# Optimization experiments

Hardware: AMD Instinct MI355X
Metric: run time of the kernel (lower is better)

Reference implementation:

```python
import jax, jax.numpy as jnp
import numpy as np

TOP_K = 5
EPS = 1e-12

def _l2norm(x, axis=-1):
    n = jnp.sqrt(jnp.sum(x * x, axis=axis, keepdims=True))
    return x / jnp.maximum(n, EPS)

def setup_inputs() -> dict:
    key = jax.random.key(0)
    ks = jax.random.split(key, 6)
    B, S, D, N = 16, 2048, 512, 200000
    return {
        "hidden_states": jax.random.normal(ks[0], (B, S, D), dtype=jnp.float32),
        "doc_embeddings": jax.random.normal(ks[1], (N, D), dtype=jnp.float32),
        "W_q": jax.random.normal(ks[2], (D, D), dtype=jnp.float32) * 0.02,
        "b_q": jnp.zeros((D,), dtype=jnp.float32),
        "W_gate": jax.random.normal(ks[3], (D, 2 * D), dtype=jnp.float32) * 0.02,
        "b_gate": jnp.zeros((D,), dtype=jnp.float32),
    }

def reference(hidden_states, doc_embeddings, W_q, b_q, W_gate, b_gate):
    B, S, D = hidden_states.shape
    # set_doc_embeddings: cosine metric normalizes doc table once
    docs = _l2norm(doc_embeddings, axis=1)          # [N, D]
    # forward: mean-pool query, linear encode
    query = hidden_states.mean(axis=1)              # [B, D]
    query = query @ W_q.T + b_q                     # torch Linear: x @ W^T + b
    # cosine similarity scan over full corpus
    q = _l2norm(query, axis=1)                      # [B, D]
    scores_full = q @ docs.T                        # [B, N]  (memory-bound scan)
    top_scores, indices = jax.lax.top_k(scores_full, TOP_K)  # [B, K], [B, K]
    # fuse context (gate method)
    retrieved = docs[indices]                       # [B, K, D] gather
    weights = jax.nn.softmax(top_scores, axis=1)    # [B, K]
    context = jnp.einsum('bk,bkd->bd', weights, retrieved)   # [B, D]
    context_exp = jnp.broadcast_to(context[:, None, :], (B, S, D))
    combined = jnp.concatenate([hidden_states, context_exp], axis=-1)  # [B, S, 2D]
    gate = jax.nn.sigmoid(combined @ W_gate.T + b_gate)       # [B, S, D]
    fused = gate * hidden_states + (1.0 - gate) * context_exp
    return top_scores, indices, fused
```

## Files before the change

kernel.cpp:

```cpp
#include <hip/hip_runtime.h>
#include <hip/hip_bf16.h>
#include <math.h>

#define BB 16
#define SS 2048
#define DD 512
#define NDOCS 200000
#define TOPK 5
#define EPSN 1e-12f
#define NEG_INF (-3.0e38f)

#define NB3 782
#define NW3 (NB3 * 4)
#define NT3 (NDOCS / 16)
#define QSTR 520

typedef short s16x8 __attribute__((ext_vector_type(8)));
typedef float f32x4 __attribute__((ext_vector_type(4)));

__device__ __forceinline__ short f2bf(float f) {
    __bf16 b = (__bf16)f;
    short s;
    __builtin_memcpy(&s, &b, 2);
    return s;
}

__device__ __forceinline__ void gload_lds16(const void* g, void* l) {
    __builtin_amdgcn_global_load_lds(
        (const __attribute__((address_space(1))) void*)g,
        (__attribute__((address_space(3))) void*)l, 16, 0, 0);
}

__global__ __launch_bounds__(128) void k1_mean_partial(
    const float* __restrict__ hs, float* __restrict__ partial) {
    int b = blockIdx.y, sc = blockIdx.x;
    int t = threadIdx.x;
    const float4* src = (const float4*)(hs + (size_t)(b * SS + sc * 64) * DD);
    float4 acc = {0.f, 0.f, 0.f, 0.f};
    for (int s = 0; s < 64; ++s) {
        float4 v = src[(size_t)s * 128 + t];
        acc.x += v.x; acc.y += v.y; acc.z += v.z; acc.w += v.w;
    }
    ((float4*)partial)[(size_t)(sc * BB + b) * 128 + t] = acc;
}

__global__ __launch_bounds__(128) void k1b_mean_reduce(
    const float* __restrict__ partial, float* __restrict__ mean) {
    int b = blockIdx.y, jc = blockIdx.x;
    int j = jc * 128 + threadIdx.x;
    float s = 0.f;
    for (int c = 0; c < 32; ++c) s += partial[(size_t)(c * BB + b) * DD + j];
    mean[(size_t)b * DD + j] = s * (1.0f / 2048.0f);
}

__global__ __launch_bounds__(256) void k2a_q_gemv(
    const float* __restrict__ mean, const float* __restrict__ Wq,
    const float* __restrict__ bq, float* __restrict__ qtmp) {
    int b = blockIdx.y, jc = blockIdx.x;
    int t = threadIdx.x;
    int r = t >> 4, c = t & 15;
    int row = jc * 16 + r;
    const float4* wr = (const float4*)(Wq + (size_t)row * DD);
    const float4* mv = (const float4*)(mean + (size_t)b * DD);
    float acc = 0.f;
#pragma unroll
    for (int it = 0; it < 8; ++it) {
        int k4 = c + it * 16;
        float4 w = wr[k4], m = mv[k4];
        acc = fmaf(w.x, m.x, acc); acc = fmaf(w.y, m.y, acc);
        acc = fmaf(w.z, m.z, acc); acc = fmaf(w.w, m.w, acc);
    }
#pragma unroll
    for (int m = 1; m < 16; m <<= 1) acc += __shfl_xor(acc, m);
    if (c == 0) qtmp[(size_t)b * DD + row] = acc + bq[row];
}

__global__ __launch_bounds__(256) void k2b_q_norm(
    const float* __restrict__ qtmp, float* __restrict__ qv) {
    int b = blockIdx.x, t = threadIdx.x;
    __shared__ float red[4];
    float a0 = qtmp[(size_t)b * DD + t];
    float a1 = qtmp[(size_t)b * DD + t + 256];
    float ss = a0 * a0 + a1 * a1;
#pragma unroll
    for (int m = 1; m < 64; m <<= 1) ss += __shfl_xor(ss, m);
    if ((t & 63) == 0) red[t >> 6] = ss;
    __syncthreads();
    float inv = 1.0f / fmaxf(sqrtf(red[0] + red[1] + red[2] + red[3]), EPSN);
    qv[(size_t)b * DD + t] = a0 * inv;
    qv[(size_t)b * DD + t + 256] = a1 * inv;
}

__global__ __launch_bounds__(256) void k3_scores(
    const float* __restrict__ docs, const float* __restrict__ qv,
    float* __restrict__ cand_s, int* __restrict__ cand_i) {
    __shared__ short qS[2][BB * QSTR];

    int t = threadIdx.x;
    int w = t >> 6, lane = t & 63;
    int bq = lane & 15, kg = lane >> 4;

    for (int u = t; u < BB * DD; u += 256) {
        int b = u >> 9, k = u & 511;
        float f = qv[u];
        unsigned uu = __float_as_uint(f);
        qS[0][b * QSTR + k] = (short)(uu >> 16);
        qS[1][b * QSTR + k] = f2bf(f - __uint_as_float(uu & 0xFFFF0000u));
    }
    __syncthreads();

    int gw = blockIdx.x * 4 + w;

    float lv[TOPK]; int li[TOPK];
#pragma unroll
    for (int r = 0; r < TOPK; ++r) { lv[r] = NEG_INF; li[r] = 0x7fffffff; }

    auto ins = [&](float s, int di) {
        if (s > lv[4] || (s == lv[4] && di < li[4])) {
            lv[4] = s; li[4] = di;
#pragma unroll
            for (int k = 4; k > 0; --k) {
                if (lv[k] > lv[k - 1] || (lv[k] == lv[k - 1] && li[k] < li[k - 1])) {
                    float tv = lv[k]; lv[k] = lv[k - 1]; lv[k - 1] = tv;
                    int   ti = li[k]; li[k] = li[k - 1]; li[k - 1] = ti;
                }
            }
        }
    };

    const short* qh_base = &qS[0][bq * QSTR + kg * 8];
    const short* ql_base = &qS[1][bq * QSTR + kg * 8];

    long tt = gw;
    const float* dpt = docs + ((long)tt * 16 + bq) * DD + kg * 8;
    f32x4 A0 = *(const f32x4*)(dpt);
    f32x4 A1 = *(const f32x4*)(dpt + 4);
    f32x4 B0 = *(const f32x4*)(dpt + 32);
    f32x4 B1 = *(const f32x4*)(dpt + 36);

    while (tt < NT3) {
        long tt2 = (tt + NW3 < NT3) ? tt + NW3 : tt;
        const float* dpn = docs + (tt2 * 16 + bq) * DD + kg * 8;

        f32x4 acc1 = {0.f, 0.f, 0.f, 0.f};
        f32x4 acc2 = {0.f, 0.f, 0.f, 0.f};
        float nrm = 0.f;

#pragma unroll
        for (int c = 0; c < 16; ++c) {
            f32x4 C0, C1;
            if (c + 2 < 16) {
                C0 = *(const f32x4*)(dpt + (c + 2) * 32);
                C1 = *(const f32x4*)(dpt + (c + 2) * 32 + 4);
            } else {
                C0 = *(const f32x4*)(dpn + (c - 14) * 32);
                C1 = *(const f32x4*)(dpn + (c - 14) * 32 + 4);
            }
            float ef[8] = {A0[0], A0[1], A0[2], A0[3], A1[0], A1[1], A1[2], A1[3]};
            s16x8 ah, al;
#pragma unroll
            for (int i = 0; i < 8; ++i) {
                unsigned u = __float_as_uint(ef[i]);
                ah[i] = (short)(u >> 16);
                al[i] = f2bf(ef[i] - __uint_as_float(u & 0xFFFF0000u));
                nrm = fmaf(ef[i], ef[i], nrm);
            }
            s16x8 qh = *(const s16x8*)(qh_base + c * 32);
            s16x8 ql = *(const s16x8*)(ql_base + c * 32);
            acc1 = __builtin_amdgcn_mfma_f32_16x16x32_bf16(ah, qh, acc1, 0, 0, 0);
            acc2 = __builtin_amdgcn_mfma_f32_16x16x32_bf16(ah, ql, acc2, 0, 0, 0);
            acc2 = __builtin_amdgcn_mfma_f32_16x16x32_bf16(al, qh, acc2, 0, 0, 0);
            A0 = B0; A1 = B1; B0 = C0; B1 = C1;
        }

        float nn = nrm + __shfl_xor(nrm, 16);
        nn += __shfl_xor(nn, 32);
        float invn = 1.0f / fmaxf(sqrtf(nn), EPSN);
        f32x4 acct = acc1 + acc2;
#pragma unroll
        for (int r = 0; r < 4; ++r) {
            float iv = __shfl(invn, kg * 4 + r);
            ins(acct[r] * iv, (int)(tt * 16 + kg * 4 + r));
        }

        tt += NW3;
        dpt = dpn;
    }

#pragma unroll
    for (int step = 16; step <= 32; step <<= 1) {
        float ov[TOPK]; int oi[TOPK];
#pragma unroll
        for (int r = 0; r < TOPK; ++r) {
            ov[r] = __shfl_xor(lv[r], step);
            oi[r] = __shfl_xor(li[r], step);
        }
#pragma unroll
        for (int r = 0; r < TOPK; ++r) ins(ov[r], oi[r]);
    }

    if (kg == 0) {
#pragma unroll
        for (int r = 0; r < TOPK; ++r) {
            cand_s[((long)gw * BB + bq) * TOPK + r] = lv[r];
            cand_i[((long)gw * BB + bq) * TOPK + r] = li[r];
        }
    }
}

__global__ __launch_bounds__(256) void k4a_topk_ctx(
    const float* __restrict__ docs, const float* __restrict__ cand_s,
    const int* __restrict__ cand_i, float* __restrict__ ctx,
    float* __restrict__ outp) {
    int b = blockIdx.x, t = threadIdx.x;
    __shared__ float sv[256];
    __shared__ int   si[256];
    __shared__ float topv[TOPK];
    __shared__ int   topi[TOPK];
    __shared__ float red[4];
    __shared__ float nrm5[TOPK];
    __shared__ float wts[TOPK];

    float lv[TOPK]; int li[TOPK];
#pragma unroll
    for (int r = 0; r < TOPK; ++r) { lv[r] = NEG_INF; li[r] = 0x7fffffff; }

    for (int j = t; j < NW3 * TOPK; j += 256) {
        int blk = j / TOPK, r = j - blk * TOPK;
        float s = cand_s[(long)blk * (BB * TOPK) + b * TOPK + r];
        int  di = cand_i[(long)blk * (BB * TOPK) + b * TOPK + r];
        if (s > lv[TOPK - 1] || (s == lv[TOPK - 1] && di < li[TOPK - 1])) {
            lv[TOPK - 1] = s; li[TOPK - 1] = di;
#pragma unroll
            for (int k = TOPK - 1; k > 0; --k) {
                if (lv[k] > lv[k - 1] || (lv[k] == lv[k - 1] && li[k] < li[k - 1])) {
                    float tv = lv[k]; lv[k] = lv[k - 1]; lv[k - 1] = tv;
                    int   ti = li[k]; li[k] = li[k - 1]; li[k - 1] = ti;
                }
            }
        }
    }

    int p = 0;
    for (int r = 0; r < TOPK; ++r) {
        float hv = (p < TOPK) ? lv[p] : NEG_INF;
        int   hi = (p < TOPK) ? li[p] : 0x7fffffff;
        sv[t] = hv; si[t] = hi;
        __syncthreads();
        for (int off = 128; off > 0; off >>= 1) {
            if (t < off) {
                float ov = sv[t + off]; int oi = si[t + off];
                if (ov > sv[t] || (ov == sv[t] && oi < si[t])) { sv[t] = ov; si[t] = oi; }
            }
            __syncthreads();
        }
        if (t == 0) { topv[r] = sv[0]; topi[r] = si[0]; }
        __syncthreads();
        if (hv == topv[r] && hi == topi[r]) ++p;
        __syncthreads();
    }

    for (int r = 0; r < TOPK; ++r) {
        const float* dr = docs + (size_t)topi[r] * DD;
        float s2 = dr[t] * dr[t] + dr[t + 256] * dr[t + 256];
#pragma unroll
        for (int m = 1; m < 64; m <<= 1) s2 += __shfl_xor(s2, m);
        if ((t & 63) == 0) red[t >> 6] = s2;
        __syncthreads();
        if (t == 0) nrm5[r] = sqrtf(red[0] + red[1] + red[2] + red[3]);
        __syncthreads();
    }

    if (t == 0) {
        float m = topv[0];
        float e[TOPK], s = 0.f;
#pragma unroll
        for (int r = 0; r < TOPK; ++r) { e[r] = expf(topv[r] - m); s += e[r]; }
#pragma unroll
        for (int r = 0; r < TOPK; ++r) wts[r] = e[r] / s;
    }
    __syncthreads();

    for (int j = t; j < DD; j += 256) {
        float c = 0.f;
#pragma unroll
        for (int r = 0; r < TOPK; ++r)
            c += wts[r] * docs[(size_t)topi[r] * DD + j] / fmaxf(nrm5[r], EPSN);
        ctx[(size_t)b * DD + j] = c;
    }

    if (t < TOPK) {
        outp[b * TOPK + t] = topv[t];
        outp[BB * TOPK + b * TOPK + t] = (float)topi[t];
    }
}

__global__ __launch_bounds__(256) void k4b_ctxb_gemv(
    const float* __restrict__ ctx, const float* __restrict__ Wg,
    const float* __restrict__ bgt, float* __restrict__ ctxb) {
    int b = blockIdx.y, jc = blockIdx.x;
    int t = threadIdx.x;
    int r = t >> 4, c = t & 15;
    int row = jc * 16 + r;
    const float4* wr = (const float4*)(Wg + (size_t)row * (2 * DD) + DD);
    const float4* mv = (const float4*)(ctx + (size_t)b * DD);
    float acc = 0.f;
#pragma unroll
    for (int it = 0; it < 8; ++it) {
        int k4 = c + it * 16;
        float4 w = wr[k4], m = mv[k4];
        acc = fmaf(w.x, m.x, acc); acc = fmaf(w.y, m.y, acc);
        acc = fmaf(w.z, m.z, acc); acc = fmaf(w.w, m.w, acc);
    }
#pragma unroll
    for (int m = 1; m < 16; m <<= 1) acc += __shfl_xor(acc, m);
    if (c == 0) ctxb[(size_t)b * DD + row] = acc + bgt[row];
}

#define BK 32
__global__ __launch_bounds__(512, 2) void k5_gemm_fused(
    const float* __restrict__ hs, const float* __restrict__ Wg,
    const float* __restrict__ ctx, const float* __restrict__ ctxb,
    float* __restrict__ outF) {
    __shared__ short At[128][BK];
    __shared__ short Bt[512][BK];
    __shared__ float ctxLds[DD];
    __shared__ float ctxbLds[DD];

    int bm = blockIdx.x;
    int t = threadIdx.x;
    int wv = t >> 6, lane = t & 63, ln = lane & 15, kg = lane >> 4;
    int wm = (wv >> 2) * 64, wn = (wv & 3) * 128;
    int bbatch = bm >> 4;

    ctxLds[t]  = ctx[(size_t)bbatch * DD + t];
    ctxbLds[t] = ctxb[(size_t)bbatch * DD + t];

    float4 pf[5][2];
    auto gload = [&](int kt) {
        {
            const float* src = hs + (size_t)(bm * 128 + (t >> 2)) * DD + kt * BK + (t & 3) * 8;
            pf[0][0] = ((const float4*)src)[0];
            pf[0][1] = ((const float4*)src)[1];
        }
#pragma unroll
        for (int i = 0; i < 4; ++i) {
            int u = t + i * 512;
            const float* src = Wg + (size_t)(u >> 2) * (2 * DD) + kt * BK + (u & 3) * 8;
            pf[1 + i][0] = ((const float4*)src)[0];
            pf[1 + i][1] = ((const float4*)src)[1];
        }
    };
    auto cvt1 = [&](float4 lo, float4 hi) {
        s16x8 cv;
        cv[0] = f2bf(lo.x); cv[1] = f2bf(lo.y); cv[2] = f2bf(lo.z); cv[3] = f2bf(lo.w);
        cv[4] = f2bf(hi.x); cv[5] = f2bf(hi.y); cv[6] = f2bf(hi.z); cv[7] = f2bf(hi.w);
        return cv;
    };
    auto cvtwrite = [&]() {
        {
            int row = t >> 2, slot = t & 3;
            int sl = slot ^ ((row >> 1) & 3);
            *(s16x8*)(&At[row][sl * 8]) = cvt1(pf[0][0], pf[0][1]);
        }
#pragma unroll
        for (int i = 0; i < 4; ++i) {
            int u = t + i * 512;
            int row = u >> 2, slot = u & 3;
            int sl = slot ^ ((row >> 1) & 3);
            *(s16x8*)(&Bt[row][sl * 8]) = cvt1(pf[1 + i][0], pf[1 + i][1]);
        }
    };

    f32x4 accv[4][8];
#pragma unroll
    for (int i = 0; i < 4; ++i)
#pragma unroll
        for (int j = 0; j < 8; ++j) accv[i][j] = (f32x4){0.f, 0.f, 0.f, 0.f};

    gload(0);
    for (int kt = 0; kt < DD / BK; ++kt) {
        __syncthreads();
        cvtwrite();
        if (kt + 1 < DD / BK) gload(kt + 1);
        __syncthreads();
        s16x8 af[4], bfr[8];
#pragma unroll
        for (int mi = 0; mi < 4; ++mi) {
            int row = wm + mi * 16 + ln;
            int sl = kg ^ ((row >> 1) & 3);
            af[mi] = *(const s16x8*)&At[row][sl * 8];
        }
#pragma unroll
        for (int nj = 0; nj < 8; ++nj) {
            int row = wn + nj * 16 + ln;
            int sl = kg ^ ((row >> 1) & 3);
            bfr[nj] = *(const s16x8*)&Bt[row][sl * 8];
        }
#pragma unroll
        for (int mi = 0; mi < 4; ++mi)
#pragma unroll
            for (int nj = 0; nj < 8; ++nj)
                accv[mi][nj] = __builtin_amdgcn_mfma_f32_16x16x32_bf16(
                    af[mi], bfr[nj], accv[mi][nj], 0, 0, 0);
    }

#pragma unroll
    for (int mi = 0; mi < 4; ++mi)
#pragma unroll
        for (int nj = 0; nj < 8; ++nj)
#pragma unroll
            for (int r = 0; r < 4; ++r) {
                int ri = wm + mi * 16 + kg * 4 + r;
                int ci = wn + nj * 16 + ln;
                size_t grow = (size_t)bm * 128 + ri;
                float logit = accv[mi][nj][r] + ctxbLds[ci];
                float g = __builtin_amdgcn_rcpf(1.0f + __expf(-logit));
                float h = hs[grow * DD + ci];
                float cx = ctxLds[ci];
                outF[grow * DD + ci] = g * h + (1.0f - g) * cx;
            }
}

extern "C" void kernel_launch(void* const* d_in, const int* in_sizes, int n_in,
                              void* d_out, int out_size, void* d_ws, size_t ws_size,
                              hipStream_t stream) {
    const float* hs   = (const float*)d_in[0];
    const float* docs = (const float*)d_in[1];
    const float* Wq   = (const float*)d_in[2];
    const float* bq   = (const float*)d_in[3];
    const float* Wg   = (const float*)d_in[4];
    const float* bgt  = (const float*)d_in[5];
    float* outp = (float*)d_out;
    float* ws = (float*)d_ws;

    float* partial = ws;
    float* mean    = partial + 32 * BB * DD;
    float* qtmp    = mean + BB * DD;
    float* qv      = qtmp + BB * DD;
    float* ctx     = qv + BB * DD;
    float* ctxb    = ctx + BB * DD;
    float* cand_s  = ctxb + BB * DD;
    int*   cand_i  = (int*)(cand_s + (size_t)NW3 * BB * TOPK);

    k1_mean_partial<<<dim3(32, BB), 128, 0, stream>>>(hs, partial);
    k1b_mean_reduce<<<dim3(4, BB), 128, 0, stream>>>(partial, mean);
    k2a_q_gemv<<<dim3(32, BB), 256, 0, stream>>>(mean, Wq, bq, qtmp);
    k2b_q_norm<<<BB, 256, 0, stream>>>(qtmp, qv);
    k3_scores<<<NB3, 256, 0, stream>>>(docs, qv, cand_s, cand_i);
    k4a_topk_ctx<<<BB, 256, 0, stream>>>(docs, cand_s, cand_i, ctx, outp);
    k4b_ctxb_gemv<<<dim3(32, BB), 256, 0, stream>>>(ctx, Wg, bgt, ctxb);
    k5_gemm_fused<<<256, 512, 0, stream>>>(hs, Wg, ctx, ctxb,
                                           outp + 2 * BB * TOPK);
}
```

Measured before the change: 257.3 us.

## Fuse small query/context kernels and deepen doc prefetch in score scan

Three small kernels (mean reduce, query GEMV, query norm) become one 16-block kernel, and the top-k/context kernel now also computes the context-gate GEMV, which removes three launches. The scoring kernel moves to 512-thread blocks with half as many blocks and prefetches four doc chunks ahead in a ring instead of two. The fused GEMVs run on only 16 blocks, with one thread walking a whole 2KB weight row through uncoalesced loads, so those phases may get slower even though launch overhead drops.

Result: slower. 289.0 us (+12.3%).

```diff
diff --git a/kernel.cpp b/kernel.cpp
--- a/kernel.cpp
+++ b/kernel.cpp
@@ -10,8 +10,8 @@
 #define EPSN 1e-12f
 #define NEG_INF (-3.0e38f)
 
-#define NB3 782
-#define NW3 (NB3 * 4)
+#define NB3 391
+#define NW3 (NB3 * 8)
 #define NT3 (NDOCS / 16)
 #define QSTR 520
 
@@ -23,12 +23,6 @@
     short s;
     __builtin_memcpy(&s, &b, 2);
     return s;
-}
-
-__device__ __forceinline__ void gload_lds16(const void* g, void* l) {
-    __builtin_amdgcn_global_load_lds(
-        (const __attribute__((address_space(1))) void*)g,
-        (__attribute__((address_space(3))) void*)l, 16, 0, 0);
 }
 
 __global__ __launch_bounds__(128) void k1_mean_partial(
@@ -44,54 +38,38 @@
     ((float4*)partial)[(size_t)(sc * BB + b) * 128 + t] = acc;
 }
 
-__global__ __launch_bounds__(128) void k1b_mean_reduce(
-    const float* __restrict__ partial, float* __restrict__ mean) {
-    int b = blockIdx.y, jc = blockIdx.x;
-    int j = jc * 128 + threadIdx.x;
+__global__ __launch_bounds__(512) void k2_query(
+    const float* __restrict__ partial, const float* __restrict__ Wq,
+    const float* __restrict__ bqv, float* __restrict__ qv) {
+    int b = blockIdx.x, t = threadIdx.x;
+    __shared__ float meanv[DD];
+    __shared__ float red[8];
     float s = 0.f;
-    for (int c = 0; c < 32; ++c) s += partial[(size_t)(c * BB + b) * DD + j];
-    mean[(size_t)b * DD + j] = s * (1.0f / 2048.0f);
-}
-
-__global__ __launch_bounds__(256) void k2a_q_gemv(
-    const float* __restrict__ mean, const float* __restrict__ Wq,
-    const float* __restrict__ bq, float* __restrict__ qtmp) {
-    int b = blockIdx.y, jc = blockIdx.x;
-    int t = threadIdx.x;
-    int r = t >> 4, c = t & 15;
-    int row = jc * 16 + r;
-    const float4* wr = (const float4*)(Wq + (size_t)row * DD);
-    const float4* mv = (const float4*)(mean + (size_t)b * DD);
-    float acc = 0.f;
-#pragma unroll
-    for (int it = 0; it < 8; ++it) {
-        int k4 = c + it * 16;
+    for (int c = 0; c < 32; ++c) s += partial[(size_t)(c * BB + b) * DD + t];
+    meanv[t] = s * (1.0f / 2048.0f);
+    __syncthreads();
+    const float4* wr = (const float4*)(Wq + (size_t)t * DD);
+    const float4* mv = (const float4*)meanv;
+    float acc = bqv[t];
+#pragma unroll 8
+    for (int k4 = 0; k4 < DD / 4; ++k4) {
         float4 w = wr[k4], m = mv[k4];
         acc = fmaf(w.x, m.x, acc); acc = fmaf(w.y, m.y, acc);
         acc = fmaf(w.z, m.z, acc); acc = fmaf(w.w, m.w, acc);
     }
-#pragma unroll
-    for (int m = 1; m < 16; m <<= 1) acc += __shfl_xor(acc, m);
-    if (c == 0) qtmp[(size_t)b * DD + row] = acc + bq[row];
-}
-
-__global__ __launch_bounds__(256) void k2b_q_norm(
-    const float* __restrict__ qtmp, float* __restrict__ qv) {
-    int b = blockIdx.x, t = threadIdx.x;
-    __shared__ float red[4];
-    float a0 = qtmp[(size_t)b * DD + t];
-    float a1 = qtmp[(size_t)b * DD + t + 256];
-    float ss = a0 * a0 + a1 * a1;
+    float ss = acc * acc;
 #pragma unroll
     for (int m = 1; m < 64; m <<= 1) ss += __shfl_xor(ss, m);
     if ((t & 63) == 0) red[t >> 6] = ss;
     __syncthreads();
-    float inv = 1.0f / fmaxf(sqrtf(red[0] + red[1] + red[2] + red[3]), EPSN);
-    qv[(size_t)b * DD + t] = a0 * inv;
-    qv[(size_t)b * DD + t + 256] = a1 * inv;
-}
-
-__global__ __launch_bounds__(256) void k3_scores(
+    float tot = 0.f;
+#pragma unroll
+    for (int i = 0; i < 8; ++i) tot += red[i];
+    float inv = 1.0f / fmaxf(sqrtf(tot), EPSN);
+    qv[(size_t)b * DD + t] = acc * inv;
+}
+
+__global__ __launch_bounds__(512) void k3_scores(
     const float* __restrict__ docs, const float* __restrict__ qv,
     float* __restrict__ cand_s, int* __restrict__ cand_i) {
     __shared__ short qS[2][BB * QSTR];
@@ -100,7 +78,7 @@
     int w = t >> 6, lane = t & 63;
     int bq = lane & 15, kg = lane >> 4;
 
-    for (int u = t; u < BB * DD; u += 256) {
+    for (int u = t; u < BB * DD; u += 512) {
         int b = u >> 9, k = u & 511;
         float f = qv[u];
         unsigned uu = __float_as_uint(f);
@@ -109,7 +87,7 @@
     }
     __syncthreads();
 
-    int gw = blockIdx.x * 4 + w;
+    int gw = blockIdx.x * 8 + w;
 
     float lv[TOPK]; int li[TOPK];
 #pragma unroll
@@ -133,10 +111,13 @@
 
     long tt = gw;
     const float* dpt = docs + ((long)tt * 16 + bq) * DD + kg * 8;
-    f32x4 A0 = *(const f32x4*)(dpt);
-    f32x4 A1 = *(const f32x4*)(dpt + 4);
-    f32x4 B0 = *(const f32x4*)(dpt + 32);
-    f32x4 B1 = *(const f32x4*)(dpt + 36);
+
+    f32x4 pa[4], pb[4];
+#pragma unroll
+    for (int i = 0; i < 4; ++i) {
+        pa[i] = *(const f32x4*)(dpt + i * 32);
+        pb[i] = *(const f32x4*)(dpt + i * 32 + 4);
+    }
 
     while (tt < NT3) {
         long tt2 = (tt + NW3 < NT3) ? tt + NW3 : tt;
@@ -148,15 +129,9 @@
 
 #pragma unroll
         for (int c = 0; c < 16; ++c) {
-            f32x4 C0, C1;
-            if (c + 2 < 16) {
-                C0 = *(const f32x4*)(dpt + (c + 2) * 32);
-                C1 = *(const f32x4*)(dpt + (c + 2) * 32 + 4);
-            } else {
-                C0 = *(const f32x4*)(dpn + (c - 14) * 32);
-                C1 = *(const f32x4*)(dpn + (c - 14) * 32 + 4);
-            }
-            float ef[8] = {A0[0], A0[1], A0[2], A0[3], A1[0], A1[1], A1[2], A1[3]};
+            const int sl = c & 3;
+            float ef[8] = {pa[sl][0], pa[sl][1], pa[sl][2], pa[sl][3],
+                           pb[sl][0], pb[sl][1], pb[sl][2], pb[sl][3]};
             s16x8 ah, al;
 #pragma unroll
             for (int i = 0; i < 8; ++i) {
@@ -170,7 +145,13 @@
             acc1 = __builtin_amdgcn_mfma_f32_16x16x32_bf16(ah, qh, acc1, 0, 0, 0);
             acc2 = __builtin_amdgcn_mfma_f32_16x16x32_bf16(ah, ql, acc2, 0, 0, 0);
             acc2 = __builtin_amdgcn_mfma_f32_16x16x32_bf16(al, qh, acc2, 0, 0, 0);
-            A0 = B0; A1 = B1; B0 = C0; B1 = C1;
+            if (c < 12) {
+                pa[sl] = *(const f32x4*)(dpt + (c + 4) * 32);
+                pb[sl] = *(const f32x4*)(dpt + (c + 4) * 32 + 4);
+            } else {
+                pa[sl] = *(const f32x4*)(dpn + (c - 12) * 32);
+                pb[sl] = *(const f32x4*)(dpn + (c - 12) * 32 + 4);
+            }
         }
 
         float nn = nrm + __shfl_xor(nrm, 16);
@@ -208,10 +189,11 @@
     }
 }
 
-__global__ __launch_bounds__(256) void k4a_topk_ctx(
-    const float* __restrict__ docs, const float* __restrict__ cand_s,
+__global__ __launch_bounds__(256) void k4_finalize(
+    const float* __restrict__ docs, const float* __restrict__ Wg,
+    const float* __restrict__ bgt, const float* __restrict__ cand_s,
     const int* __restrict__ cand_i, float* __restrict__ ctx,
-    float* __restrict__ outp) {
+    float* __restrict__ ctxb, float* __restrict__ outp) {
     int b = blockIdx.x, t = threadIdx.x;
     __shared__ float sv[256];
     __shared__ int   si[256];
@@ -220,6 +202,7 @@
     __shared__ float red[4];
     __shared__ float nrm5[TOPK];
     __shared__ float wts[TOPK];
+    __shared__ float ctxLds[DD];
 
     float lv[TOPK]; int li[TOPK];
 #pragma unroll
@@ -286,35 +269,30 @@
 #pragma unroll
         for (int r = 0; r < TOPK; ++r)
             c += wts[r] * docs[(size_t)topi[r] * DD + j] / fmaxf(nrm5[r], EPSN);
+        ctxLds[j] = c;
         ctx[(size_t)b * DD + j] = c;
+    }
+    __syncthreads();
+
+    const float4* cv = (const float4*)ctxLds;
+#pragma unroll
+    for (int rr = 0; rr < 2; ++rr) {
+        int row = t + rr * 256;
+        const float4* wr = (const float4*)(Wg + (size_t)row * (2 * DD) + DD);
+        float acc = bgt[row];
+#pragma unroll 8
+        for (int k4 = 0; k4 < DD / 4; ++k4) {
+            float4 wv = wr[k4], mv = cv[k4];
+            acc = fmaf(wv.x, mv.x, acc); acc = fmaf(wv.y, mv.y, acc);
+            acc = fmaf(wv.z, mv.z, acc); acc = fmaf(wv.w, mv.w, acc);
+        }
+        ctxb[(size_t)b * DD + row] = acc;
     }
 
     if (t < TOPK) {
         outp[b * TOPK + t] = topv[t];
         outp[BB * TOPK + b * TOPK + t] = (float)topi[t];
     }
-}
-
-__global__ __launch_bounds__(256) void k4b_ctxb_gemv(
-    const float* __restrict__ ctx, const float* __restrict__ Wg,
-    const float* __restrict__ bgt, float* __restrict__ ctxb) {
-    int b = blockIdx.y, jc = blockIdx.x;
-    int t = threadIdx.x;
-    int r = t >> 4, c = t & 15;
-    int row = jc * 16 + r;
-    const float4* wr = (const float4*)(Wg + (size_t)row * (2 * DD) + DD);
-    const float4* mv = (const float4*)(ctx + (size_t)b * DD);
-    float acc = 0.f;
-#pragma unroll
-    for (int it = 0; it < 8; ++it) {
-        int k4 = c + it * 16;
-        float4 w = wr[k4], m = mv[k4];
-        acc = fmaf(w.x, m.x, acc); acc = fmaf(w.y, m.y, acc);
-        acc = fmaf(w.z, m.z, acc); acc = fmaf(w.w, m.w, acc);
-    }
-#pragma unroll
-    for (int m = 1; m < 16; m <<= 1) acc += __shfl_xor(acc, m);
-    if (c == 0) ctxb[(size_t)b * DD + row] = acc + bgt[row];
 }
 
 #define BK 32
@@ -435,21 +413,17 @@
     float* ws = (float*)d_ws;
 
     float* partial = ws;
-    float* mean    = partial + 32 * BB * DD;
-    float* qtmp    = mean + BB * DD;
-    float* qv      = qtmp + BB * DD;
+    float* qv      = partial + 32 * BB * DD;
     float* ctx     = qv + BB * DD;
     float* ctxb    = ctx + BB * DD;
     float* cand_s  = ctxb + BB * DD;
     int*   cand_i  = (int*)(cand_s + (size_t)NW3 * BB * TOPK);
 
     k1_mean_partial<<<dim3(32, BB), 128, 0, stream>>>(hs, partial);
-    k1b_mean_reduce<<<dim3(4, BB), 128, 0, stream>>>(partial, mean);
-    k2a_q_gemv<<<dim3(32, BB), 256, 0, stream>>>(mean, Wq, bq, qtmp);
-    k2b_q_norm<<<BB, 256, 0, stream>>>(qtmp, qv);
-    k3_scores<<<NB3, 256, 0, stream>>>(docs, qv, cand_s, cand_i);
-    k4a_topk_ctx<<<BB, 256, 0, stream>>>(docs, cand_s, cand_i, ctx, outp);
-    k4b_ctxb_gemv<<<dim3(32, BB), 256, 0, stream>>>(ctx, Wg, bgt, ctxb);
+    k2_query<<<BB, 512, 0, stream>>>(partial, Wq, bq, qv);
+    k3_scores<<<NB3, 512, 0, stream>>>(docs, qv, cand_s, cand_i);
+    k4_finalize<<<BB, 256, 0, stream>>>(docs, Wg, bgt, cand_s, cand_i,
+                                        ctx, ctxb, outp);
     k5_gemm_fused<<<256, 512, 0, stream>>>(hs, Wg, ctx, ctxb,
                                            outp + 2 * BB * TOPK);
 }
```
